# Kernel optimization log

Hardware: AMD Instinct MI355X
Metric: run time of the kernel (lower is better)

The kernel has to match this reference:

```python
import jax, jax.numpy as jnp
import numpy as np

B, T, IN, H = 512, 2048, 2, 128


def setup_inputs() -> dict:
    key = jax.random.key(0)
    ks = jax.random.split(key, 14)
    u = lambda k, shape: jax.random.uniform(k, shape, jnp.float32, -0.1, 0.1)
    return {
        "x": jax.random.normal(ks[0], (B, T, IN), jnp.float32),
        "mask": jnp.ones((B, T), jnp.float32),
        "emb_W": u(ks[1], (H, IN)), "emb_b": u(ks[2], (H,)),
        "enc_W": u(ks[3], (H, H)), "enc_b": u(ks[4], (H,)),
        "dec_input": u(ks[5], (H,)), "Vec": u(ks[6], (H,)),
        "Wq_W": u(ks[7], (H, H)), "Wq_b": u(ks[8], (H,)),
        "Wref_W": u(ks[9], (H, H)), "Wref_b": u(ks[10], (H,)),
        "fc1_W": u(ks[11], (H, H)), "fc2_W": u(ks[12], (2, H)),
    }


def reference(x, mask, emb_W, emb_b, enc_W, enc_b, dec_input, Vec,
              Wq_W, Wq_b, Wref_W, Wref_b, fc1_W, fc2_W):
    # Embedding: (B,T,IN) -> (B,T,H)
    x_embed = jnp.einsum("bti,hi->bth", x, emb_W) + emb_b
    # Encoder (stand-in for external Encoder class): per-token Linear + mask
    ref = (jnp.einsum("bti,hi->bth", x_embed, enc_W) + enc_b) * mask[:, :, None]

    def glimpse(query, ref):
        # query: (B,H); ref: (B,T,H)
        u1 = query @ Wq_W.T + Wq_b                                  # (B,H)
        # Conv1d kernel size 1 == pointwise linear over hidden dim
        u2 = jnp.einsum("bti,oi->bot", ref, Wref_W) + Wref_b[None, :, None]  # (B,H,T)
        u = jnp.einsum("h,bht->bt", Vec, jnp.tanh(u1[:, :, None] + u2))      # (B,T)
        a = jax.nn.softmax(u, axis=1)                               # (B,T)
        return jnp.einsum("bht,bt->bh", u2, a)                      # (B,H)

    query = jnp.broadcast_to(dec_input, (x.shape[0], dec_input.shape[0]))
    for _ in range(2):
        query = glimpse(query, ref)

    # final2FC: Linear(no bias) -> ReLU -> Linear(no bias); squeeze(-1) twice is a no-op (last dim=2)
    pred_l = jax.nn.relu(query @ fc1_W.T) @ fc2_W.T                 # (B,2)
    return pred_l
```

## Files before the change

### kernel.cpp

```cpp
#include <hip/hip_runtime.h>
#include <hip/hip_bf16.h>


#define Bsz 512
#define Tsz 2048
#define Hsz 128
#define TPB 512
#define TOK 4

#define C2LOG2E 2.8853900817779268f
#define LOG2E   1.4426950408889634f

__device__ __forceinline__ float exp2fast(float x) { return __builtin_amdgcn_exp2f(x); }
__device__ __forceinline__ float rcpfast(float x)  { return __builtin_amdgcn_rcpf(x); }

__global__ __launch_bounds__(128) void kprep(
        const float* __restrict__ embW, const float* __restrict__ embB,
        const float* __restrict__ encW, const float* __restrict__ encB,
        const float* __restrict__ wrefW, const float* __restrict__ wrefB,
        const float* __restrict__ wqW, const float* __restrict__ wqB,
        const float* __restrict__ dec, const float* __restrict__ vec,
        float4* __restrict__ SC, float4* __restrict__ UC, float* __restrict__ V2) {
    __shared__ float m0[Hsz], m1[Hsz], cc[Hsz], dq[Hsz];
    int h = threadIdx.x;
    float a0 = 0.f, a1 = 0.f, ac = 0.f;
    for (int k = 0; k < Hsz; ++k) {
        float w = encW[h * Hsz + k];
        a0 = fmaf(w, embW[2 * k + 0], a0);
        a1 = fmaf(w, embW[2 * k + 1], a1);
        ac = fmaf(w, embB[k], ac);
    }
    m0[h] = a0; m1[h] = a1; cc[h] = ac + encB[h]; dq[h] = dec[h];
    __syncthreads();
    float p0 = 0.f, p1 = 0.f, pe = 0.f, uq = wqB[h];
    for (int k = 0; k < Hsz; ++k) {
        float w = wrefW[h * Hsz + k];
        p0 = fmaf(w, m0[k], p0);
        p1 = fmaf(w, m1[k], p1);
        pe = fmaf(w, cc[k], pe);
        uq = fmaf(wqW[h * Hsz + k], dq[k], uq);
    }
    float wb = wrefB[h];
    SC[h] = make_float4(C2LOG2E * p0, C2LOG2E * p1, C2LOG2E * pe, C2LOG2E * (uq + wb));
    UC[h] = make_float4(p0, p1, pe, wb);
    V2[h] = 2.f * vec[h];
}

__global__ __launch_bounds__(TPB) void kfused(
        const float* __restrict__ x, const float* __restrict__ mask,
        const float4* __restrict__ SC, const float4* __restrict__ UC,
        const float* __restrict__ V2,
        const float* __restrict__ wqW, const float* __restrict__ wqB,
        const float* __restrict__ fc1, const float* __restrict__ fc2,
        float* __restrict__ out) {
    __shared__ float4 cf[Hsz];
    __shared__ float4 uc[Hsz];
    __shared__ float v2s[Hsz];
    __shared__ float q[Hsz], rr[Hsz];
    __shared__ float pp[4][Hsz];
    __shared__ float redm[8];
    __shared__ float4 red4[8];
    __shared__ float4 tripS;

    int b = blockIdx.x, tid = threadIdx.x;
    int wave = tid >> 6, lane = tid & 63;
    if (tid < Hsz) { cf[tid] = SC[tid]; uc[tid] = UC[tid]; v2s[tid] = V2[tid]; }

    float2 xv[TOK]; float mk[TOK];
    const float2* x2 = (const float2*)(x + (size_t)b * Tsz * 2);
    const float* mrow = mask + (size_t)b * Tsz;
    #pragma unroll
    for (int j = 0; j < TOK; ++j) { xv[j] = x2[j * TPB + tid]; mk[j] = mrow[j * TPB + tid]; }
    __syncthreads();

    float X0 = 0.f, X1 = 0.f, Cm = 0.f;
    #pragma unroll 1
    for (int g = 0; g < 2; ++g) {
        float acc[TOK];
        #pragma unroll
        for (int j = 0; j < TOK; ++j) acc[j] = 0.f;
        for (int h = 0; h < Hsz; ++h) {
            float4 cv = cf[h]; float vv = v2s[h];
            #pragma unroll
            for (int j = 0; j < TOK; ++j) {
                float w = fmaf(xv[j].x, cv.x, fmaf(xv[j].y, cv.y, cv.z));
                float a = fmaf(mk[j], w, cv.w);
                float r = rcpfast(exp2fast(a) + 1.f);
                acc[j] = fmaf(vv, r, acc[j]);
            }
        }
        float am = fminf(fminf(acc[0], acc[1]), fminf(acc[2], acc[3]));
        for (int off = 32; off; off >>= 1) am = fminf(am, __shfl_xor(am, off));
        if (lane == 0) redm[wave] = am;
        __syncthreads();
        am = redm[0];
        #pragma unroll
        for (int w2 = 1; w2 < 8; ++w2) am = fminf(am, redm[w2]);
        float Z = 0.f, Sm = 0.f, S0 = 0.f, S1 = 0.f;
        #pragma unroll
        for (int j = 0; j < TOK; ++j) {
            float e = exp2fast((am - acc[j]) * LOG2E);
            float em = e * mk[j];
            Z += e; Sm += em;
            S0 = fmaf(em, xv[j].x, S0);
            S1 = fmaf(em, xv[j].y, S1);
        }
        for (int off = 32; off; off >>= 1) {
            Z += __shfl_xor(Z, off); Sm += __shfl_xor(Sm, off);
            S0 += __shfl_xor(S0, off); S1 += __shfl_xor(S1, off);
        }
        if (lane == 0) red4[wave] = make_float4(Z, Sm, S0, S1);
        __syncthreads();
        if (tid == 0) {
            float Zt = 0.f, Smt = 0.f, S0t = 0.f, S1t = 0.f;
            #pragma unroll
            for (int w2 = 0; w2 < 8; ++w2) {
                Zt += red4[w2].x; Smt += red4[w2].y; S0t += red4[w2].z; S1t += red4[w2].w;
            }
            float inv = 1.f / Zt;
            tripS = make_float4(S0t * inv, S1t * inv, Smt * inv, 0.f);
        }
        __syncthreads();
        X0 = tripS.x; X1 = tripS.y; Cm = tripS.z;

        if (g == 0) {
            if (tid < Hsz) {
                float4 u4 = uc[tid];
                q[tid] = fmaf(X0, u4.x, fmaf(X1, u4.y, fmaf(Cm, u4.z, u4.w)));
            }
            __syncthreads();
            {
                int h = tid & (Hsz - 1), part = tid >> 7;
                float s = 0.f;
                const float* wr = wqW + (size_t)h * Hsz + part * 32;
                #pragma unroll 8
                for (int k = 0; k < 32; ++k) s = fmaf(wr[k], q[part * 32 + k], s);
                pp[part][h] = s;
            }
            __syncthreads();
            if (tid < Hsz) {
                float u1h = wqB[tid] + ((pp[0][tid] + pp[1][tid]) + (pp[2][tid] + pp[3][tid]));
                float4 c4 = cf[tid];
                c4.w = C2LOG2E * (u1h + uc[tid].w);
                cf[tid] = c4;
            }
            __syncthreads();
        }
    }
    if (tid < Hsz) {
        float4 u4 = uc[tid];
        q[tid] = fmaf(X0, u4.x, fmaf(X1, u4.y, fmaf(Cm, u4.z, u4.w)));
    }
    __syncthreads();
    {
        int h = tid & (Hsz - 1), part = tid >> 7;
        float s = 0.f;
        const float* fr = fc1 + (size_t)h * Hsz + part * 32;
        #pragma unroll 8
        for (int k = 0; k < 32; ++k) s = fmaf(fr[k], q[part * 32 + k], s);
        pp[part][h] = s;
    }
    __syncthreads();
    if (tid < Hsz) {
        rr[tid] = fmaxf(0.f, (pp[0][tid] + pp[1][tid]) + (pp[2][tid] + pp[3][tid]));
    }
    __syncthreads();
    if (tid < 128) {
        int o = tid >> 6, l = tid & 63;
        float s = fc2[o * Hsz + l] * rr[l] + fc2[o * Hsz + 64 + l] * rr[64 + l];
        for (int off = 32; off; off >>= 1) s += __shfl_xor(s, off);
        if (l == 0) out[b * 2 + o] = s;
    }
}

extern "C" void kernel_launch(void* const* d_in, const int* in_sizes, int n_in,
                              void* d_out, int out_size, void* d_ws, size_t ws_size,
                              hipStream_t stream) {
    const float* x     = (const float*)d_in[0];
    const float* mask  = (const float*)d_in[1];
    const float* embW  = (const float*)d_in[2];
    const float* embB  = (const float*)d_in[3];
    const float* encW  = (const float*)d_in[4];
    const float* encB  = (const float*)d_in[5];
    const float* dec   = (const float*)d_in[6];
    const float* vec   = (const float*)d_in[7];
    const float* wqW   = (const float*)d_in[8];
    const float* wqB   = (const float*)d_in[9];
    const float* wrefW = (const float*)d_in[10];
    const float* wrefB = (const float*)d_in[11];
    const float* fc1   = (const float*)d_in[12];
    const float* fc2   = (const float*)d_in[13];

    float* ws = (float*)d_ws;
    float4* SC = (float4*)ws;
    float4* UC = (float4*)(ws + 512);
    float* V2  = ws + 1024;
    float* out = (float*)d_out;

    kprep<<<1, 128, 0, stream>>>(embW, embB, encW, encB, wrefW, wrefB, wqW, wqB,
                                 dec, vec, SC, UC, V2);
    kfused<<<Bsz, TPB, 0, stream>>>(x, mask, SC, UC, V2, wqW, wqB, fc1, fc2, out);
}
```

Before: 84.57 us.

## Double block size, halve tokens per thread, use readlane for Vec weights

```diff
diff --git a/kernel.cpp b/kernel.cpp
--- a/kernel.cpp
+++ b/kernel.cpp
@@ -5,14 +5,17 @@
 #define Bsz 512
 #define Tsz 2048
 #define Hsz 128
-#define TPB 512
-#define TOK 4
+#define TPB 1024
+#define TOK 2
 
 #define C2LOG2E 2.8853900817779268f
 #define LOG2E   1.4426950408889634f
 
 __device__ __forceinline__ float exp2fast(float x) { return __builtin_amdgcn_exp2f(x); }
 __device__ __forceinline__ float rcpfast(float x)  { return __builtin_amdgcn_rcpf(x); }
+__device__ __forceinline__ float readlanef(float v, int l) {
+    return __uint_as_float(__builtin_amdgcn_readlane(__float_as_uint(v), l));
+}
 
 __global__ __launch_bounds__(128) void kprep(
         const float* __restrict__ embW, const float* __restrict__ embB,
@@ -20,7 +23,7 @@
         const float* __restrict__ wrefW, const float* __restrict__ wrefB,
         const float* __restrict__ wqW, const float* __restrict__ wqB,
         const float* __restrict__ dec, const float* __restrict__ vec,
-        float4* __restrict__ SC, float4* __restrict__ UC, float* __restrict__ V2) {
+        float4* __restrict__ SC, float* __restrict__ V2G, float4* __restrict__ UC) {
     __shared__ float m0[Hsz], m1[Hsz], cc[Hsz], dq[Hsz];
     int h = threadIdx.x;
     float a0 = 0.f, a1 = 0.f, ac = 0.f;
@@ -41,84 +44,85 @@
         uq = fmaf(wqW[h * Hsz + k], dq[k], uq);
     }
     float wb = wrefB[h];
-    SC[h] = make_float4(C2LOG2E * p0, C2LOG2E * p1, C2LOG2E * pe, C2LOG2E * (uq + wb));
-    UC[h] = make_float4(p0, p1, pe, wb);
-    V2[h] = 2.f * vec[h];
-}
-
-__global__ __launch_bounds__(TPB) void kfused(
+    SC[h]  = make_float4(C2LOG2E * p0, C2LOG2E * p1, C2LOG2E * pe, C2LOG2E * (uq + wb));
+    V2G[h] = 2.f * vec[h];
+    UC[h]  = make_float4(p0, p1, pe, wb);
+}
+
+__global__ __launch_bounds__(TPB, 8) void kfused(
         const float* __restrict__ x, const float* __restrict__ mask,
-        const float4* __restrict__ SC, const float4* __restrict__ UC,
-        const float* __restrict__ V2,
+        const float4* __restrict__ SC, const float* __restrict__ V2G,
+        const float4* __restrict__ UC,
         const float* __restrict__ wqW, const float* __restrict__ wqB,
         const float* __restrict__ fc1, const float* __restrict__ fc2,
         float* __restrict__ out) {
     __shared__ float4 cf[Hsz];
     __shared__ float4 uc[Hsz];
-    __shared__ float v2s[Hsz];
     __shared__ float q[Hsz], rr[Hsz];
-    __shared__ float pp[4][Hsz];
-    __shared__ float redm[8];
-    __shared__ float4 red4[8];
+    __shared__ float pp[8][Hsz];
+    __shared__ float4 red4[16];
     __shared__ float4 tripS;
 
     int b = blockIdx.x, tid = threadIdx.x;
     int wave = tid >> 6, lane = tid & 63;
-    if (tid < Hsz) { cf[tid] = SC[tid]; uc[tid] = UC[tid]; v2s[tid] = V2[tid]; }
-
-    float2 xv[TOK]; float mk[TOK];
+    if (tid < Hsz) { cf[tid] = SC[tid]; uc[tid] = UC[tid]; }
+    float vvA = V2G[lane], vvB = V2G[64 + lane];
+
     const float2* x2 = (const float2*)(x + (size_t)b * Tsz * 2);
     const float* mrow = mask + (size_t)b * Tsz;
+    float xm0[TOK], xm1[TOK], mk[TOK], xr0[TOK], xr1[TOK];
     #pragma unroll
-    for (int j = 0; j < TOK; ++j) { xv[j] = x2[j * TPB + tid]; mk[j] = mrow[j * TPB + tid]; }
+    for (int j = 0; j < TOK; ++j) {
+        float2 xv = x2[j * TPB + tid];
+        float m = mrow[j * TPB + tid];
+        mk[j] = m; xr0[j] = xv.x; xr1[j] = xv.y;
+        xm0[j] = xv.x * m; xm1[j] = xv.y * m;
+    }
     __syncthreads();
 
     float X0 = 0.f, X1 = 0.f, Cm = 0.f;
     #pragma unroll 1
     for (int g = 0; g < 2; ++g) {
-        float acc[TOK];
-        #pragma unroll
-        for (int j = 0; j < TOK; ++j) acc[j] = 0.f;
-        for (int h = 0; h < Hsz; ++h) {
-            float4 cv = cf[h]; float vv = v2s[h];
-            #pragma unroll
-            for (int j = 0; j < TOK; ++j) {
-                float w = fmaf(xv[j].x, cv.x, fmaf(xv[j].y, cv.y, cv.z));
-                float a = fmaf(mk[j], w, cv.w);
-                float r = rcpfast(exp2fast(a) + 1.f);
-                acc[j] = fmaf(vv, r, acc[j]);
-            }
-        }
-        float am = fminf(fminf(acc[0], acc[1]), fminf(acc[2], acc[3]));
-        for (int off = 32; off; off >>= 1) am = fminf(am, __shfl_xor(am, off));
-        if (lane == 0) redm[wave] = am;
-        __syncthreads();
-        am = redm[0];
-        #pragma unroll
-        for (int w2 = 1; w2 < 8; ++w2) am = fminf(am, redm[w2]);
-        float Z = 0.f, Sm = 0.f, S0 = 0.f, S1 = 0.f;
-        #pragma unroll
-        for (int j = 0; j < TOK; ++j) {
-            float e = exp2fast((am - acc[j]) * LOG2E);
-            float em = e * mk[j];
-            Z += e; Sm += em;
-            S0 = fmaf(em, xv[j].x, S0);
-            S1 = fmaf(em, xv[j].y, S1);
-        }
+        float acc0 = 0.f, acc1 = 0.f;
+        #pragma unroll 8
+        for (int h = 0; h < 64; ++h) {
+            float4 cv = cf[h];
+            float vv = readlanef(vvA, h);
+            float a0 = fmaf(xm0[0], cv.x, fmaf(xm1[0], cv.y, fmaf(mk[0], cv.z, cv.w)));
+            acc0 = fmaf(vv, rcpfast(exp2fast(a0) + 1.f), acc0);
+            float a1 = fmaf(xm0[1], cv.x, fmaf(xm1[1], cv.y, fmaf(mk[1], cv.z, cv.w)));
+            acc1 = fmaf(vv, rcpfast(exp2fast(a1) + 1.f), acc1);
+        }
+        #pragma unroll 8
+        for (int h = 64; h < 128; ++h) {
+            float4 cv = cf[h];
+            float vv = readlanef(vvB, h - 64);
+            float a0 = fmaf(xm0[0], cv.x, fmaf(xm1[0], cv.y, fmaf(mk[0], cv.z, cv.w)));
+            acc0 = fmaf(vv, rcpfast(exp2fast(a0) + 1.f), acc0);
+            float a1 = fmaf(xm0[1], cv.x, fmaf(xm1[1], cv.y, fmaf(mk[1], cv.z, cv.w)));
+            acc1 = fmaf(vv, rcpfast(exp2fast(a1) + 1.f), acc1);
+        }
+        float e0 = exp2fast(-LOG2E * acc0), e1 = exp2fast(-LOG2E * acc1);
+        float em0 = e0 * mk[0], em1 = e1 * mk[1];
+        float Z = e0 + e1, Sm = em0 + em1;
+        float S0 = fmaf(em0, xr0[0], em1 * xr0[1]);
+        float S1 = fmaf(em0, xr1[0], em1 * xr1[1]);
         for (int off = 32; off; off >>= 1) {
             Z += __shfl_xor(Z, off); Sm += __shfl_xor(Sm, off);
             S0 += __shfl_xor(S0, off); S1 += __shfl_xor(S1, off);
         }
         if (lane == 0) red4[wave] = make_float4(Z, Sm, S0, S1);
         __syncthreads();
-        if (tid == 0) {
-            float Zt = 0.f, Smt = 0.f, S0t = 0.f, S1t = 0.f;
-            #pragma unroll
-            for (int w2 = 0; w2 < 8; ++w2) {
-                Zt += red4[w2].x; Smt += red4[w2].y; S0t += red4[w2].z; S1t += red4[w2].w;
-            }
-            float inv = 1.f / Zt;
-            tripS = make_float4(S0t * inv, S1t * inv, Smt * inv, 0.f);
+        if (tid < 16) {
+            float4 v = red4[tid];
+            for (int off = 8; off; off >>= 1) {
+                v.x += __shfl_xor(v.x, off); v.y += __shfl_xor(v.y, off);
+                v.z += __shfl_xor(v.z, off); v.w += __shfl_xor(v.w, off);
+            }
+            if (tid == 0) {
+                float inv = 1.f / v.x;
+                tripS = make_float4(v.z * inv, v.w * inv, v.y * inv, 0.f);
+            }
         }
         __syncthreads();
         X0 = tripS.x; X1 = tripS.y; Cm = tripS.z;
@@ -132,17 +136,17 @@
             {
                 int h = tid & (Hsz - 1), part = tid >> 7;
                 float s = 0.f;
-                const float* wr = wqW + (size_t)h * Hsz + part * 32;
-                #pragma unroll 8
-                for (int k = 0; k < 32; ++k) s = fmaf(wr[k], q[part * 32 + k], s);
+                const float* wr = wqW + (size_t)h * Hsz + part * 16;
+                #pragma unroll
+                for (int k = 0; k < 16; ++k) s = fmaf(wr[k], q[part * 16 + k], s);
                 pp[part][h] = s;
             }
             __syncthreads();
             if (tid < Hsz) {
-                float u1h = wqB[tid] + ((pp[0][tid] + pp[1][tid]) + (pp[2][tid] + pp[3][tid]));
-                float4 c4 = cf[tid];
-                c4.w = C2LOG2E * (u1h + uc[tid].w);
-                cf[tid] = c4;
+                float u1h = wqB[tid];
+                #pragma unroll
+                for (int p = 0; p < 8; ++p) u1h += pp[p][tid];
+                cf[tid].w = C2LOG2E * (u1h + uc[tid].w);
             }
             __syncthreads();
         }
@@ -155,14 +159,17 @@
     {
         int h = tid & (Hsz - 1), part = tid >> 7;
         float s = 0.f;
-        const float* fr = fc1 + (size_t)h * Hsz + part * 32;
-        #pragma unroll 8
-        for (int k = 0; k < 32; ++k) s = fmaf(fr[k], q[part * 32 + k], s);
+        const float* fr = fc1 + (size_t)h * Hsz + part * 16;
+        #pragma unroll
+        for (int k = 0; k < 16; ++k) s = fmaf(fr[k], q[part * 16 + k], s);
         pp[part][h] = s;
     }
     __syncthreads();
     if (tid < Hsz) {
-        rr[tid] = fmaxf(0.f, (pp[0][tid] + pp[1][tid]) + (pp[2][tid] + pp[3][tid]));
+        float s = 0.f;
+        #pragma unroll
+        for (int p = 0; p < 8; ++p) s += pp[p][tid];
+        rr[tid] = fmaxf(0.f, s);
     }
     __syncthreads();
     if (tid < 128) {
@@ -194,10 +201,10 @@
     float* ws = (float*)d_ws;
     float4* SC = (float4*)ws;
     float4* UC = (float4*)(ws + 512);
-    float* V2  = ws + 1024;
+    float* V2G = ws + 1024;
     float* out = (float*)d_out;
 
     kprep<<<1, 128, 0, stream>>>(embW, embB, encW, encB, wrefW, wrefB, wqW, wqB,
-                                 dec, vec, SC, UC, V2);
-    kfused<<<Bsz, TPB, 0, stream>>>(x, mask, SC, UC, V2, wqW, wqB, fc1, fc2, out);
-}
+                                 dec, vec, SC, V2G, UC);
+    kfused<<<Bsz, TPB, 0, stream>>>(x, mask, SC, V2G, UC, wqW, wqB, fc1, fc2, out);
+}
```

Result: slower. 94.42 us (+11.6%).

## Split fused glimpse kernel into per-chunk scoring kernels with readlane coefficient broadcast

Applied to the files above, without the earlier changes.

```diff
diff --git a/kernel.cpp b/kernel.cpp
--- a/kernel.cpp
+++ b/kernel.cpp
@@ -5,14 +5,19 @@
 #define Bsz 512
 #define Tsz 2048
 #define Hsz 128
-#define TPB 512
+#define THR 128
 #define TOK 4
+#define QB 4
+static_assert(QB * THR * TOK == Tsz, "token tiling must cover each row exactly");
 
 #define C2LOG2E 2.8853900817779268f
 #define LOG2E   1.4426950408889634f
 
 __device__ __forceinline__ float exp2fast(float x) { return __builtin_amdgcn_exp2f(x); }
 __device__ __forceinline__ float rcpfast(float x)  { return __builtin_amdgcn_rcpf(x); }
+__device__ __forceinline__ float readlanef(float v, int l) {
+    return __uint_as_float(__builtin_amdgcn_readlane(__float_as_uint(v), l));
+}
 
 __global__ __launch_bounds__(128) void kprep(
         const float* __restrict__ embW, const float* __restrict__ embB,
@@ -20,7 +25,7 @@
         const float* __restrict__ wrefW, const float* __restrict__ wrefB,
         const float* __restrict__ wqW, const float* __restrict__ wqB,
         const float* __restrict__ dec, const float* __restrict__ vec,
-        float4* __restrict__ SC, float4* __restrict__ UC, float* __restrict__ V2) {
+        float4* __restrict__ SCA, float4* __restrict__ UC, float* __restrict__ V2G) {
     __shared__ float m0[Hsz], m1[Hsz], cc[Hsz], dq[Hsz];
     int h = threadIdx.x;
     float a0 = 0.f, a1 = 0.f, ac = 0.f;
@@ -41,136 +46,132 @@
         uq = fmaf(wqW[h * Hsz + k], dq[k], uq);
     }
     float wb = wrefB[h];
-    SC[h] = make_float4(C2LOG2E * p0, C2LOG2E * p1, C2LOG2E * pe, C2LOG2E * (uq + wb));
-    UC[h] = make_float4(p0, p1, pe, wb);
-    V2[h] = 2.f * vec[h];
-}
-
-__global__ __launch_bounds__(TPB) void kfused(
+    SCA[h] = make_float4(C2LOG2E * p0, C2LOG2E * p1, C2LOG2E * pe, C2LOG2E * (uq + wb));
+    UC[h]  = make_float4(p0, p1, pe, wb);
+    V2G[h] = 2.f * vec[h];
+}
+
+__global__ __launch_bounds__(THR) void kscore(
         const float* __restrict__ x, const float* __restrict__ mask,
-        const float4* __restrict__ SC, const float4* __restrict__ UC,
-        const float* __restrict__ V2,
+        const float4* __restrict__ quadG, int bstride,
+        const float* __restrict__ V2G,
+        float4* __restrict__ statsOut) {
+    __shared__ float4 wr2[2];
+    int blk = blockIdx.x, tid = threadIdx.x;
+    int b = blk >> 2, qb = blk & 3;
+    int wave = tid >> 6, lane = tid & 63;
+
+    const float4* qbase = quadG + (size_t)b * bstride;
+    float4 qa  = qbase[lane];
+    float4 qb4 = qbase[64 + lane];
+    float  va  = V2G[lane], vb = V2G[64 + lane];
+
+    size_t tok0 = (size_t)b * Tsz + (size_t)qb * (THR * TOK);
+    const float4* x4 = (const float4*)(x + tok0 * 2);
+    float4 xa = x4[tid * 2], xb = x4[tid * 2 + 1];
+    float4 m4 = ((const float4*)(mask + tok0))[tid];
+    float mk[TOK]  = {m4.x, m4.y, m4.z, m4.w};
+    float xm0[TOK] = {xa.x * m4.x, xa.z * m4.y, xb.x * m4.z, xb.z * m4.w};
+    float xm1[TOK] = {xa.y * m4.x, xa.w * m4.y, xb.y * m4.z, xb.w * m4.w};
+    float acc[TOK] = {0.f, 0.f, 0.f, 0.f};
+
+    #pragma unroll 8
+    for (int h = 0; h < 64; ++h) {
+        float A = readlanef(qa.x, h), Bc = readlanef(qa.y, h);
+        float Cc = readlanef(qa.z, h), D = readlanef(qa.w, h);
+        float vv = readlanef(va, h);
+        #pragma unroll
+        for (int j = 0; j < TOK; ++j) {
+            float a = fmaf(xm0[j], A, fmaf(xm1[j], Bc, fmaf(mk[j], Cc, D)));
+            acc[j] = fmaf(vv, rcpfast(exp2fast(a) + 1.f), acc[j]);
+        }
+    }
+    #pragma unroll 8
+    for (int h = 0; h < 64; ++h) {
+        float A = readlanef(qb4.x, h), Bc = readlanef(qb4.y, h);
+        float Cc = readlanef(qb4.z, h), D = readlanef(qb4.w, h);
+        float vv = readlanef(vb, h);
+        #pragma unroll
+        for (int j = 0; j < TOK; ++j) {
+            float a = fmaf(xm0[j], A, fmaf(xm1[j], Bc, fmaf(mk[j], Cc, D)));
+            acc[j] = fmaf(vv, rcpfast(exp2fast(a) + 1.f), acc[j]);
+        }
+    }
+
+    float Z = 0.f, Sm = 0.f, S0 = 0.f, S1 = 0.f;
+    #pragma unroll
+    for (int j = 0; j < TOK; ++j) {
+        float e = exp2fast(-LOG2E * acc[j]);
+        Z += e;
+        Sm = fmaf(e, mk[j], Sm);
+        S0 = fmaf(e, xm0[j], S0);
+        S1 = fmaf(e, xm1[j], S1);
+    }
+    for (int off = 32; off; off >>= 1) {
+        Z += __shfl_xor(Z, off); Sm += __shfl_xor(Sm, off);
+        S0 += __shfl_xor(S0, off); S1 += __shfl_xor(S1, off);
+    }
+    if (lane == 0) wr2[wave] = make_float4(Z, Sm, S0, S1);
+    __syncthreads();
+    if (tid == 0) {
+        float4 u = wr2[0], v = wr2[1];
+        statsOut[blk] = make_float4(u.x + v.x, u.y + v.y, u.z + v.z, u.w + v.w);
+    }
+}
+
+__global__ __launch_bounds__(THR) void kmid(
+        const float4* __restrict__ statsA, const float4* __restrict__ UC,
+        const float4* __restrict__ SCA,
         const float* __restrict__ wqW, const float* __restrict__ wqB,
+        float4* __restrict__ QB1) {
+    __shared__ float q[Hsz];
+    int b = blockIdx.x, tid = threadIdx.x;
+    float Z = 0.f, Sm = 0.f, S0 = 0.f, S1 = 0.f;
+    #pragma unroll
+    for (int i = 0; i < QB; ++i) {
+        float4 t = statsA[b * QB + i];
+        Z += t.x; Sm += t.y; S0 += t.z; S1 += t.w;
+    }
+    float inv = 1.f / Z;
+    float X0 = S0 * inv, X1 = S1 * inv, Cm = Sm * inv;
+    float4 u4 = UC[tid];
+    q[tid] = fmaf(X0, u4.x, fmaf(X1, u4.y, fmaf(Cm, u4.z, u4.w)));
+    __syncthreads();
+    float s = wqB[tid];
+    const float* wr = wqW + (size_t)tid * Hsz;
+    #pragma unroll 8
+    for (int k = 0; k < Hsz; ++k) s = fmaf(wr[k], q[k], s);
+    float4 sc = SCA[tid];
+    QB1[b * Hsz + tid] = make_float4(sc.x, sc.y, sc.z, C2LOG2E * (s + u4.w));
+}
+
+__global__ __launch_bounds__(THR) void kfin(
+        const float4* __restrict__ statsB, const float4* __restrict__ UC,
         const float* __restrict__ fc1, const float* __restrict__ fc2,
         float* __restrict__ out) {
-    __shared__ float4 cf[Hsz];
-    __shared__ float4 uc[Hsz];
-    __shared__ float v2s[Hsz];
     __shared__ float q[Hsz], rr[Hsz];
-    __shared__ float pp[4][Hsz];
-    __shared__ float redm[8];
-    __shared__ float4 red4[8];
-    __shared__ float4 tripS;
-
     int b = blockIdx.x, tid = threadIdx.x;
-    int wave = tid >> 6, lane = tid & 63;
-    if (tid < Hsz) { cf[tid] = SC[tid]; uc[tid] = UC[tid]; v2s[tid] = V2[tid]; }
-
-    float2 xv[TOK]; float mk[TOK];
-    const float2* x2 = (const float2*)(x + (size_t)b * Tsz * 2);
-    const float* mrow = mask + (size_t)b * Tsz;
+    float Z = 0.f, Sm = 0.f, S0 = 0.f, S1 = 0.f;
     #pragma unroll
-    for (int j = 0; j < TOK; ++j) { xv[j] = x2[j * TPB + tid]; mk[j] = mrow[j * TPB + tid]; }
-    __syncthreads();
-
-    float X0 = 0.f, X1 = 0.f, Cm = 0.f;
-    #pragma unroll 1
-    for (int g = 0; g < 2; ++g) {
-        float acc[TOK];
-        #pragma unroll
-        for (int j = 0; j < TOK; ++j) acc[j] = 0.f;
-        for (int h = 0; h < Hsz; ++h) {
-            float4 cv = cf[h]; float vv = v2s[h];
-            #pragma unroll
-            for (int j = 0; j < TOK; ++j) {
-                float w = fmaf(xv[j].x, cv.x, fmaf(xv[j].y, cv.y, cv.z));
-                float a = fmaf(mk[j], w, cv.w);
-                float r = rcpfast(exp2fast(a) + 1.f);
-                acc[j] = fmaf(vv, r, acc[j]);
-            }
-        }
-        float am = fminf(fminf(acc[0], acc[1]), fminf(acc[2], acc[3]));
-        for (int off = 32; off; off >>= 1) am = fminf(am, __shfl_xor(am, off));
-        if (lane == 0) redm[wave] = am;
-        __syncthreads();
-        am = redm[0];
-        #pragma unroll
-        for (int w2 = 1; w2 < 8; ++w2) am = fminf(am, redm[w2]);
-        float Z = 0.f, Sm = 0.f, S0 = 0.f, S1 = 0.f;
-        #pragma unroll
-        for (int j = 0; j < TOK; ++j) {
-            float e = exp2fast((am - acc[j]) * LOG2E);
-            float em = e * mk[j];
-            Z += e; Sm += em;
-            S0 = fmaf(em, xv[j].x, S0);
-            S1 = fmaf(em, xv[j].y, S1);
-        }
-        for (int off = 32; off; off >>= 1) {
-            Z += __shfl_xor(Z, off); Sm += __shfl_xor(Sm, off);
-            S0 += __shfl_xor(S0, off); S1 += __shfl_xor(S1, off);
-        }
-        if (lane == 0) red4[wave] = make_float4(Z, Sm, S0, S1);
-        __syncthreads();
-        if (tid == 0) {
-            float Zt = 0.f, Smt = 0.f, S0t = 0.f, S1t = 0.f;
-            #pragma unroll
-            for (int w2 = 0; w2 < 8; ++w2) {
-                Zt += red4[w2].x; Smt += red4[w2].y; S0t += red4[w2].z; S1t += red4[w2].w;
-            }
-            float inv = 1.f / Zt;
-            tripS = make_float4(S0t * inv, S1t * inv, Smt * inv, 0.f);
-        }
-        __syncthreads();
-        X0 = tripS.x; X1 = tripS.y; Cm = tripS.z;
-
-        if (g == 0) {
-            if (tid < Hsz) {
-                float4 u4 = uc[tid];
-                q[tid] = fmaf(X0, u4.x, fmaf(X1, u4.y, fmaf(Cm, u4.z, u4.w)));
-            }
-            __syncthreads();
-            {
-                int h = tid & (Hsz - 1), part = tid >> 7;
-                float s = 0.f;
-                const float* wr = wqW + (size_t)h * Hsz + part * 32;
-                #pragma unroll 8
-                for (int k = 0; k < 32; ++k) s = fmaf(wr[k], q[part * 32 + k], s);
-                pp[part][h] = s;
-            }
-            __syncthreads();
-            if (tid < Hsz) {
-                float u1h = wqB[tid] + ((pp[0][tid] + pp[1][tid]) + (pp[2][tid] + pp[3][tid]));
-                float4 c4 = cf[tid];
-                c4.w = C2LOG2E * (u1h + uc[tid].w);
-                cf[tid] = c4;
-            }
-            __syncthreads();
-        }
-    }
-    if (tid < Hsz) {
-        float4 u4 = uc[tid];
-        q[tid] = fmaf(X0, u4.x, fmaf(X1, u4.y, fmaf(Cm, u4.z, u4.w)));
-    }
-    __syncthreads();
-    {
-        int h = tid & (Hsz - 1), part = tid >> 7;
-        float s = 0.f;
-        const float* fr = fc1 + (size_t)h * Hsz + part * 32;
-        #pragma unroll 8
-        for (int k = 0; k < 32; ++k) s = fmaf(fr[k], q[part * 32 + k], s);
-        pp[part][h] = s;
-    }
-    __syncthreads();
-    if (tid < Hsz) {
-        rr[tid] = fmaxf(0.f, (pp[0][tid] + pp[1][tid]) + (pp[2][tid] + pp[3][tid]));
-    }
-    __syncthreads();
-    if (tid < 128) {
-        int o = tid >> 6, l = tid & 63;
-        float s = fc2[o * Hsz + l] * rr[l] + fc2[o * Hsz + 64 + l] * rr[64 + l];
-        for (int off = 32; off; off >>= 1) s += __shfl_xor(s, off);
-        if (l == 0) out[b * 2 + o] = s;
-    }
+    for (int i = 0; i < QB; ++i) {
+        float4 t = statsB[b * QB + i];
+        Z += t.x; Sm += t.y; S0 += t.z; S1 += t.w;
+    }
+    float inv = 1.f / Z;
+    float X0 = S0 * inv, X1 = S1 * inv, Cm = Sm * inv;
+    float4 u4 = UC[tid];
+    q[tid] = fmaf(X0, u4.x, fmaf(X1, u4.y, fmaf(Cm, u4.z, u4.w)));
+    __syncthreads();
+    float s = 0.f;
+    const float* fr = fc1 + (size_t)tid * Hsz;
+    #pragma unroll 8
+    for (int k = 0; k < Hsz; ++k) s = fmaf(fr[k], q[k], s);
+    rr[tid] = fmaxf(s, 0.f);
+    __syncthreads();
+    int o = tid >> 6, l = tid & 63;
+    float s2 = fc2[o * Hsz + l] * rr[l] + fc2[o * Hsz + 64 + l] * rr[64 + l];
+    for (int off = 32; off; off >>= 1) s2 += __shfl_xor(s2, off);
+    if (l == 0) out[b * 2 + o] = s2;
 }
 
 extern "C" void kernel_launch(void* const* d_in, const int* in_sizes, int n_in,
@@ -192,12 +193,18 @@
     const float* fc2   = (const float*)d_in[13];
 
     float* ws = (float*)d_ws;
-    float4* SC = (float4*)ws;
-    float4* UC = (float4*)(ws + 512);
-    float* V2  = ws + 1024;
+    float4* SCA    = (float4*)(ws + 0);
+    float4* UC     = (float4*)(ws + 512);
+    float*  V2G    = ws + 1024;
+    float4* QB1    = (float4*)(ws + 1536);
+    float4* statsA = (float4*)(ws + 263680);
+    float4* statsB = (float4*)(ws + 271872);
     float* out = (float*)d_out;
 
     kprep<<<1, 128, 0, stream>>>(embW, embB, encW, encB, wrefW, wrefB, wqW, wqB,
-                                 dec, vec, SC, UC, V2);
-    kfused<<<Bsz, TPB, 0, stream>>>(x, mask, SC, UC, V2, wqW, wqB, fc1, fc2, out);
-}
+                                 dec, vec, SCA, UC, V2G);
+    kscore<<<Bsz * QB, THR, 0, stream>>>(x, mask, SCA, 0, V2G, statsA);
+    kmid<<<Bsz, THR, 0, stream>>>(statsA, UC, SCA, wqW, wqB, QB1);
+    kscore<<<Bsz * QB, THR, 0, stream>>>(x, mask, QB1, Hsz, V2G, statsB);
+    kfin<<<Bsz, THR, 0, stream>>>(statsB, UC, fc1, fc2, out);
+}
```

Result: slower. 110.7 us (+30.9%).
